# Optimization experiments

Measured on AMD Instinct MI355X. Metric: run time of the kernel, lower is better.

Reference implementation:

```python
import jax, jax.numpy as jnp
import numpy as np

B, TED, G, N, E, MD, NOISE = 10000, 512, 64, 2000, 64000, 15, 128
PAC = 10
PACDIM = (TED + NOISE) * PAC  # 6400
D0, D1 = 1024, 512


def _linear_params(k, fan_in, fan_out):
    kw, kb = jax.random.split(k)
    lim = 1.0 / np.sqrt(fan_in)
    w = jax.random.uniform(kw, (fan_in, fan_out), minval=-lim, maxval=lim, dtype=jnp.float32)
    b = jax.random.uniform(kb, (fan_out,), minval=-lim, maxval=lim, dtype=jnp.float32)
    return w, b


def setup_inputs() -> dict:
    key = jax.random.key(0)
    ks = jax.random.split(key, 12)
    inp = {
        'input_': jax.random.normal(ks[0], (B, TED), dtype=jnp.float32),
        'graphs_x': jax.random.normal(ks[1], (G, N, 1), dtype=jnp.float32),
        'edge_index': jax.random.randint(ks[2], (G, 2, E), 0, N, dtype=jnp.int32),
        'graph_ids': jax.random.randint(ks[3], (B,), 0, G, dtype=jnp.int32),
        'chain': jax.random.normal(ks[4], (B, 1), dtype=jnp.float32),
        'metadata': jax.random.normal(ks[5], (B, MD), dtype=jnp.float32),
    }
    inp['gcn_w'], inp['gcn_b'] = _linear_params(ks[6], 1, 1)
    inp['meta_w'], inp['meta_b'] = _linear_params(ks[7], 1 + MD, 32)
    inp['gme_w'], inp['gme_b'] = _linear_params(ks[8], N + 32, NOISE)
    inp['seq_w0'], inp['seq_b0'] = _linear_params(ks[9], PACDIM, D0)
    inp['seq_w1'], inp['seq_b1'] = _linear_params(ks[10], D0, D1)
    inp['seq_w2'], inp['seq_b2'] = _linear_params(ks[11], D1, 1)
    return inp


def _gcn_one(x, ei, gcn_w, gcn_b):
    # GCNConv(1,1) with self-loops and symmetric normalization.
    loops = jnp.arange(N, dtype=ei.dtype)
    src = jnp.concatenate([ei[0], loops])
    dst = jnp.concatenate([ei[1], loops])
    deg = jax.ops.segment_sum(jnp.ones_like(src, dtype=x.dtype), dst, num_segments=N)
    dinv = jax.lax.rsqrt(deg)  # deg >= 1 due to self-loops
    norm = dinv[src] * dinv[dst]  # [E+N]
    xw = x @ gcn_w  # [N,1]
    msg = xw[src] * norm[:, None]
    out = jax.ops.segment_sum(msg, dst, num_segments=N) + gcn_b
    return out.reshape(-1)  # flatten -> [N]


def reference(input_, graphs_x, edge_index, graph_ids, chain, metadata,
              gcn_w, gcn_b, meta_w, meta_b, gme_w, gme_b,
              seq_w0, seq_b0, seq_w1, seq_b1, seq_w2, seq_b2):
    # per-unique-graph GCN, vectorized over G graphs
    gcn_out = jax.vmap(lambda x, ei: _gcn_one(x, ei, gcn_w, gcn_b))(graphs_x, edge_index)  # [G,N]
    graph_emb = gcn_out[graph_ids]  # gather: [B,N]
    all_meta = jnp.concatenate([chain, metadata], axis=1)  # [B,1+MD]
    meta_emb = jax.nn.relu(all_meta @ meta_w + meta_b)  # [B,32]
    noise = jnp.concatenate([graph_emb, meta_emb], axis=1) @ gme_w + gme_b  # [B,NOISE]
    h = jnp.concatenate([input_, noise], axis=1).reshape(-1, PACDIM)  # [B/PAC, PACDIM]
    h = jax.nn.leaky_relu(h @ seq_w0 + seq_b0, 0.2)  # dropout omitted (eval mode)
    h = jax.nn.leaky_relu(h @ seq_w1 + seq_b1, 0.2)
    return h @ seq_w2 + seq_b2  # [B/PAC, 1]
```

## Files before the change

kernel.cpp:

```cpp
#include <hip/hip_runtime.h>

typedef __bf16 bf16_t;
typedef __bf16 bf16x4 __attribute__((ext_vector_type(4)));
typedef __bf16 bf16x8 __attribute__((ext_vector_type(8)));
typedef float floatx4 __attribute__((ext_vector_type(4)));

#define G_GRAPHS 64
#define N_NODES 2000
#define N_EDGES 64000
#define BATCH 10000
#define TED_ 512
#define NOISE_ 128
#define PACDIM_ 6400
#define D0_ 1024
#define D1_ 512
#define MROWS 1000
#define ESPLIT 8
#define EPB (N_EDGES / ESPLIT)

__device__ __forceinline__ void glds16(const void* g, void* l) {
    __builtin_amdgcn_global_load_lds(
        (__attribute__((address_space(1))) void*)(g),
        (__attribute__((address_space(3))) void*)(l), 16, 0, 0);
}

__global__ __launch_bounds__(256) void zero_kernel(float4* __restrict__ p, int n4) {
    int i = blockIdx.x * 256 + threadIdx.x;
    if (i < n4) p[i] = make_float4(0.f, 0.f, 0.f, 0.f);
}

__global__ __launch_bounds__(512) void deg_kernel(
    const int* __restrict__ edge_index, float* __restrict__ degs)
{
    __shared__ float h[N_NODES];
    const int g = blockIdx.y, s = blockIdx.x, tid = threadIdx.x;
    for (int n = tid; n < N_NODES; n += 512) h[n] = 0.f;
    __syncthreads();
    const int* dst = edge_index + (size_t)g * 2 * N_EDGES + N_EDGES + s * EPB;
    for (int e = tid; e < EPB; e += 512) atomicAdd(&h[dst[e]], 1.0f);
    __syncthreads();
    float* dg = degs + (size_t)g * N_NODES;
    for (int n = tid; n < N_NODES; n += 512) {
        float v = h[n];
        if (v != 0.f) atomicAdd(&dg[n], v);
    }
}

__global__ __launch_bounds__(512) void msg_kernel(
    const float* __restrict__ graphs_x, const int* __restrict__ edge_index,
    const float* __restrict__ degs, float* __restrict__ outs)
{
    __shared__ float xsl[N_NODES];
    __shared__ float dvl[N_NODES];
    __shared__ float oh[N_NODES];
    const int g = blockIdx.y, s = blockIdx.x, tid = threadIdx.x;
    const float* xg = graphs_x + (size_t)g * N_NODES;
    const float* dgg = degs + (size_t)g * N_NODES;
    for (int n = tid; n < N_NODES; n += 512) {
        xsl[n] = xg[n];
        dvl[n] = rsqrtf(dgg[n] + 1.0f);
        oh[n] = 0.f;
    }
    __syncthreads();
    const int* src = edge_index + (size_t)g * 2 * N_EDGES + s * EPB;
    const int* dst = src + N_EDGES;
    for (int e = tid; e < EPB; e += 512) {
        int ss = src[e], dd = dst[e];
        atomicAdd(&oh[dd], xsl[ss] * dvl[ss] * dvl[dd]);
    }
    __syncthreads();
    float* og = outs + (size_t)g * N_NODES;
    for (int n = tid; n < N_NODES; n += 512) {
        float v = oh[n];
        if (v != 0.f) atomicAdd(&og[n], v);
    }
}

__global__ __launch_bounds__(512) void gnoise_kernel(
    const float* __restrict__ graphs_x, const float* __restrict__ degs,
    const float* __restrict__ outs,
    const float* __restrict__ gcn_w, const float* __restrict__ gcn_b,
    const float* __restrict__ gme_w, float* __restrict__ gnoise)
{
    __shared__ float of[N_NODES];
    __shared__ float part[4][128];
    const int g = blockIdx.x, tid = threadIdx.x;
    const float w = gcn_w[0], b = gcn_b[0];
    for (int n = tid; n < N_NODES; n += 512) {
        float di2 = 1.0f / (degs[(size_t)g * N_NODES + n] + 1.0f);
        of[n] = w * (outs[(size_t)g * N_NODES + n]
                     + graphs_x[(size_t)g * N_NODES + n] * di2) + b;
    }
    __syncthreads();
    const int j = tid & 127, ch = tid >> 7;
    float acc = 0.f;
    const int n0 = ch * 500;
    for (int n = n0; n < n0 + 500; n++)
        acc += of[n] * gme_w[(size_t)n * 128 + j];
    part[ch][j] = acc;
    __syncthreads();
    if (tid < 128)
        gnoise[(size_t)g * 128 + tid] =
            part[0][tid] + part[1][tid] + part[2][tid] + part[3][tid];
}

__global__ __launch_bounds__(256) void pack_input_kernel(
    const float* __restrict__ in, bf16_t* __restrict__ A)
{
    int idx = blockIdx.x * 256 + threadIdx.x;
    if (idx >= BATCH * TED_ / 4) return;
    float4 v = ((const float4*)in)[idx];
    int b = idx >> 7;
    int c = (idx & 127) << 2;
    int r = b / 10, slot = b - r * 10;
    bf16x4 o = { (bf16_t)v.x, (bf16_t)v.y, (bf16_t)v.z, (bf16_t)v.w };
    *(bf16x4*)(A + (size_t)r * PACDIM_ + slot * 640 + c) = o;
}

__global__ __launch_bounds__(256) void meta_noise_kernel(
    const float* __restrict__ chain, const float* __restrict__ metadata,
    const int* __restrict__ graph_ids,
    const float* __restrict__ meta_w, const float* __restrict__ meta_b,
    const float* __restrict__ gme_w, const float* __restrict__ gme_b,
    const float* __restrict__ gnoise, bf16_t* __restrict__ A)
{
    int wid = (blockIdx.x * 256 + threadIdx.x) >> 6;
    int lane = threadIdx.x & 63;
    if (wid >= BATCH) return;
    const int b = wid;
    float me = 0.f;
    if (lane < 32) {
        me = meta_b[lane] + chain[b] * meta_w[lane];
        for (int i = 1; i < 16; i++)
            me += metadata[(size_t)b * 15 + (i - 1)] * meta_w[(size_t)i * 32 + lane];
        me = me > 0.f ? me : 0.f;
    }
    const int gid = graph_ids[b];
    const int j1 = lane, j2 = lane + 64;
    float n1 = gnoise[(size_t)gid * 128 + j1] + gme_b[j1];
    float n2 = gnoise[(size_t)gid * 128 + j2] + gme_b[j2];
    for (int k = 0; k < 32; k++) {
        float mk = __shfl(me, k, 64);
        const float* wrow = gme_w + (size_t)(N_NODES + k) * 128;
        n1 += mk * wrow[j1];
        n2 += mk * wrow[j2];
    }
    int r = b / 10, slot = b - r * 10;
    bf16_t* dp = A + (size_t)r * PACDIM_ + slot * 640 + TED_;
    dp[j1] = (bf16_t)n1;
    dp[j2] = (bf16_t)n2;
}

__global__ __launch_bounds__(256) void transpose_bf16_kernel(
    const float* __restrict__ W, bf16_t* __restrict__ Wt, int R, int C)
{
    __shared__ float t[32][33];
    int c0 = blockIdx.x * 32, r0 = blockIdx.y * 32;
    int tx = threadIdx.x & 31, ty = threadIdx.x >> 5;
    for (int yy = ty; yy < 32; yy += 8)
        t[yy][tx] = W[(size_t)(r0 + yy) * C + c0 + tx];
    __syncthreads();
    for (int yy = ty; yy < 32; yy += 8)
        Wt[(size_t)(c0 + yy) * R + r0 + tx] = (bf16_t)t[tx][yy];
}

__global__ __launch_bounds__(256) void gemm_bt_splitk_kernel(
    const bf16_t* __restrict__ A,
    const bf16_t* __restrict__ Bt,
    float* __restrict__ P,
    int M, int N, int K, int KS)
{
    __shared__ __align__(16) bf16_t As[128 * 32];
    __shared__ __align__(16) bf16_t Bs[128 * 32];
    const int tid = threadIdx.x;
    const int wave = tid >> 6;
    const int lane = tid & 63;
    const int mBase = blockIdx.y * 128;
    const int nBase = blockIdx.x * 128;
    const int z = blockIdx.z;
    const int Mp = gridDim.y * 128;
    const int wm = (wave & 1) * 64;
    const int wn = (wave >> 1) * 64;

    floatx4 acc[4][4] = {};

    const int c0 = tid, c1 = tid + 256;
    const int rA0 = c0 >> 2, k80 = (c0 & 3) * 8;
    const int rA1 = c1 >> 2, k81 = (c1 & 3) * 8;
    int gm0 = mBase + rA0; if (gm0 > M - 1) gm0 = M - 1;
    int gm1 = mBase + rA1; if (gm1 > M - 1) gm1 = M - 1;
    const bf16_t* aP0 = A + (size_t)gm0 * K + k80;
    const bf16_t* aP1 = A + (size_t)gm1 * K + k81;
    const bf16_t* bP0 = Bt + (size_t)(nBase + rA0) * K + k80;
    const bf16_t* bP1 = Bt + (size_t)(nBase + rA1) * K + k81;
    char* lA0 = (char*)As + wave * 1024;
    char* lA1 = (char*)As + 4096 + wave * 1024;
    char* lB0 = (char*)Bs + wave * 1024;
    char* lB1 = (char*)Bs + 4096 + wave * 1024;

    const int kq = (lane >> 4) * 8;
    const int mr = lane & 15;
    const bf16x8* ra[4]; const bf16x8* rb[4];
    for (int i = 0; i < 4; i++)
        ra[i] = (const bf16x8*)&As[(wm + i * 16 + mr) * 32 + kq];
    for (int j = 0; j < 4; j++)
        rb[j] = (const bf16x8*)&Bs[(wn + j * 16 + mr) * 32 + kq];

    const int kEnd = z * KS + KS;
    for (int k0 = z * KS; k0 < kEnd; k0 += 32) {
        __syncthreads();
        glds16(aP0 + k0, lA0);
        glds16(aP1 + k0, lA1);
        glds16(bP0 + k0, lB0);
        glds16(bP1 + k0, lB1);
        __syncthreads();
        bf16x8 af[4], bfr[4];
        for (int i = 0; i < 4; i++) af[i] = *ra[i];
        for (int j = 0; j < 4; j++) bfr[j] = *rb[j];
        for (int i = 0; i < 4; i++)
            for (int j = 0; j < 4; j++)
                acc[i][j] = __builtin_amdgcn_mfma_f32_16x16x32_bf16(
                    af[i], bfr[j], acc[i][j], 0, 0, 0);
    }

    float* Pz = P + (size_t)z * Mp * N;
    const int rq = (lane >> 4) * 4;
    const int cn = lane & 15;
    for (int j = 0; j < 4; j++) {
        int col = nBase + wn + j * 16 + cn;
        for (int i = 0; i < 4; i++)
            for (int r = 0; r < 4; r++) {
                int rowm = mBase + wm + i * 16 + rq + r;
                Pz[(size_t)rowm * N + col] = acc[i][j][r];
            }
    }
}

__global__ __launch_bounds__(256) void reduce_bias_leaky_kernel(
    const float* __restrict__ P, const float* __restrict__ bias,
    bf16_t* __restrict__ C, int M, int N, int Mp, int S)
{
    int idx = blockIdx.x * 256 + threadIdx.x;
    int total = M * (N >> 2);
    if (idx >= total) return;
    int nv = N >> 2;
    int r = idx / nv, c4 = (idx - r * nv) << 2;
    size_t off = (size_t)r * N + c4;
    size_t stride = (size_t)Mp * N;
    float4 v = *(const float4*)(P + off);
    for (int s = 1; s < S; s++) {
        float4 u = *(const float4*)(P + s * stride + off);
        v.x += u.x; v.y += u.y; v.z += u.z; v.w += u.w;
    }
    const float4 bv = *(const float4*)(bias + c4);
    v.x += bv.x; v.y += bv.y; v.z += bv.z; v.w += bv.w;
    v.x = v.x > 0.f ? v.x : 0.2f * v.x;
    v.y = v.y > 0.f ? v.y : 0.2f * v.y;
    v.z = v.z > 0.f ? v.z : 0.2f * v.z;
    v.w = v.w > 0.f ? v.w : 0.2f * v.w;
    bf16x4 o = { (bf16_t)v.x, (bf16_t)v.y, (bf16_t)v.z, (bf16_t)v.w };
    *(bf16x4*)(C + off) = o;
}

__global__ __launch_bounds__(256) void final_kernel(
    const bf16_t* __restrict__ H2, const float* __restrict__ w2,
    const float* __restrict__ b2, float* __restrict__ out)
{
    int wid = (blockIdx.x * 256 + threadIdx.x) >> 6;
    int lane = threadIdx.x & 63;
    if (wid >= MROWS) return;
    const bf16_t* row = H2 + (size_t)wid * D1_;
    float s = 0.f;
    for (int i = 0; i < 8; i++) {
        int c = i * 64 + lane;
        s += (float)row[c] * w2[c];
    }
    for (int off = 32; off; off >>= 1) s += __shfl_down(s, off, 64);
    if (lane == 0) out[wid] = s + b2[0];
}

extern "C" void kernel_launch(void* const* d_in, const int* in_sizes, int n_in,
                              void* d_out, int out_size, void* d_ws, size_t ws_size,
                              hipStream_t stream)
{
    const float* input_    = (const float*)d_in[0];
    const float* graphs_x  = (const float*)d_in[1];
    const int*   edge_idx  = (const int*)  d_in[2];
    const int*   graph_ids = (const int*)  d_in[3];
    const float* chain     = (const float*)d_in[4];
    const float* metadata  = (const float*)d_in[5];
    const float* gcn_w     = (const float*)d_in[6];
    const float* gcn_b     = (const float*)d_in[7];
    const float* meta_w    = (const float*)d_in[8];
    const float* meta_b    = (const float*)d_in[9];
    const float* gme_w     = (const float*)d_in[10];
    const float* gme_b     = (const float*)d_in[11];
    const float* seq_w0    = (const float*)d_in[12];
    const float* seq_b0    = (const float*)d_in[13];
    const float* seq_w1    = (const float*)d_in[14];
    const float* seq_b1    = (const float*)d_in[15];
    const float* seq_w2    = (const float*)d_in[16];
    const float* seq_b2    = (const float*)d_in[17];
    float* out = (float*)d_out;

    char* ws = (char*)d_ws;
    float*  gnoise = (float*)(ws + 0);
    float*  degs   = (float*)(ws + 32768);
    float*  outs   = (float*)(ws + 544768);
    bf16_t* Abuf   = (bf16_t*)(ws + 1056768);
    bf16_t* W0t    = (bf16_t*)(ws + 13856768);
    bf16_t* W1t    = (bf16_t*)(ws + 26963968);
    bf16_t* H1     = (bf16_t*)(ws + 28012544);
    bf16_t* H2     = (bf16_t*)(ws + 30060544);
    float*  P      = (float*)(ws + 31084544);

    zero_kernel<<<(2 * G_GRAPHS * N_NODES / 4 + 255) / 256, 256, 0, stream>>>(
        (float4*)degs, 2 * G_GRAPHS * N_NODES / 4);
    deg_kernel<<<dim3(ESPLIT, G_GRAPHS), 512, 0, stream>>>(edge_idx, degs);
    msg_kernel<<<dim3(ESPLIT, G_GRAPHS), 512, 0, stream>>>(graphs_x, edge_idx, degs, outs);
    gnoise_kernel<<<G_GRAPHS, 512, 0, stream>>>(graphs_x, degs, outs, gcn_w, gcn_b,
                                                gme_w, gnoise);

    pack_input_kernel<<<(BATCH * TED_ / 4 + 255) / 256, 256, 0, stream>>>(input_, Abuf);
    meta_noise_kernel<<<(BATCH * 64 + 255) / 256, 256, 0, stream>>>(
        chain, metadata, graph_ids, meta_w, meta_b, gme_w, gme_b, gnoise, Abuf);
    transpose_bf16_kernel<<<dim3(D0_ / 32, PACDIM_ / 32), 256, 0, stream>>>(
        seq_w0, W0t, PACDIM_, D0_);
    transpose_bf16_kernel<<<dim3(D1_ / 32, D0_ / 32), 256, 0, stream>>>(
        seq_w1, W1t, D0_, D1_);

    gemm_bt_splitk_kernel<<<dim3(D0_ / 128, 8, 4), 256, 0, stream>>>(
        Abuf, W0t, P, MROWS, D0_, PACDIM_, 1600);
    reduce_bias_leaky_kernel<<<(MROWS * D0_ / 4 + 255) / 256, 256, 0, stream>>>(
        P, seq_b0, H1, MROWS, D0_, 1024, 4);

    gemm_bt_splitk_kernel<<<dim3(D1_ / 128, 8, 8), 256, 0, stream>>>(
        H1, W1t, P, MROWS, D1_, D0_, 128);
    reduce_bias_leaky_kernel<<<(MROWS * D1_ / 4 + 255) / 256, 256, 0, stream>>>(
        P, seq_b1, H2, MROWS, D1_, 1024, 8);

    final_kernel<<<(MROWS * 64 + 255) / 256, 256, 0, stream>>>(H2, seq_w2, seq_b2, out);
}
```

Baseline: 302.2 us.

## Fuse small kernels, split gnoise across blocks, raise GEMM0 split-K

The gnoise projection now runs as 4 node chunks per graph and accumulates with atomics, giving more blocks and more parallelism. The input packing and meta/noise kernels are merged into one launch. The layer-1 reduce, bias and leaky ReLU are folded into the final dot-product kernel, which drops the H2 buffer. The first GEMM's split-K goes from 4 to 8. Together these cut launch count and increase parallelism, at the cost of larger partial-sum traffic and extra reads in the final kernel.

```diff
diff --git a/kernel.cpp b/kernel.cpp
--- a/kernel.cpp
+++ b/kernel.cpp
@@ -17,6 +17,8 @@
 #define MROWS 1000
 #define ESPLIT 8
 #define EPB (N_EDGES / ESPLIT)
+#define S0 8
+#define S1 8
 
 __device__ __forceinline__ void glds16(const void* g, void* l) {
     __builtin_amdgcn_global_load_lds(
@@ -76,55 +78,55 @@
     }
 }
 
-__global__ __launch_bounds__(512) void gnoise_kernel(
+__global__ __launch_bounds__(512) void gnoise_part_kernel(
     const float* __restrict__ graphs_x, const float* __restrict__ degs,
     const float* __restrict__ outs,
     const float* __restrict__ gcn_w, const float* __restrict__ gcn_b,
     const float* __restrict__ gme_w, float* __restrict__ gnoise)
 {
-    __shared__ float of[N_NODES];
+    __shared__ float of[500];
     __shared__ float part[4][128];
-    const int g = blockIdx.x, tid = threadIdx.x;
+    const int s = blockIdx.x, g = blockIdx.y, tid = threadIdx.x;
+    const int nBase = s * 500;
     const float w = gcn_w[0], b = gcn_b[0];
-    for (int n = tid; n < N_NODES; n += 512) {
-        float di2 = 1.0f / (degs[(size_t)g * N_NODES + n] + 1.0f);
-        of[n] = w * (outs[(size_t)g * N_NODES + n]
-                     + graphs_x[(size_t)g * N_NODES + n] * di2) + b;
+    for (int n = tid; n < 500; n += 512) {
+        int gn = nBase + n;
+        float di2 = 1.0f / (degs[(size_t)g * N_NODES + gn] + 1.0f);
+        of[n] = w * (outs[(size_t)g * N_NODES + gn]
+                     + graphs_x[(size_t)g * N_NODES + gn] * di2) + b;
     }
     __syncthreads();
     const int j = tid & 127, ch = tid >> 7;
     float acc = 0.f;
-    const int n0 = ch * 500;
-    for (int n = n0; n < n0 + 500; n++)
-        acc += of[n] * gme_w[(size_t)n * 128 + j];
+    const int n0 = ch * 125;
+    for (int n = n0; n < n0 + 125; n++)
+        acc += of[n] * gme_w[(size_t)(nBase + n) * 128 + j];
     part[ch][j] = acc;
     __syncthreads();
     if (tid < 128)
-        gnoise[(size_t)g * 128 + tid] =
-            part[0][tid] + part[1][tid] + part[2][tid] + part[3][tid];
-}
-
-__global__ __launch_bounds__(256) void pack_input_kernel(
-    const float* __restrict__ in, bf16_t* __restrict__ A)
-{
-    int idx = blockIdx.x * 256 + threadIdx.x;
-    if (idx >= BATCH * TED_ / 4) return;
-    float4 v = ((const float4*)in)[idx];
-    int b = idx >> 7;
-    int c = (idx & 127) << 2;
-    int r = b / 10, slot = b - r * 10;
-    bf16x4 o = { (bf16_t)v.x, (bf16_t)v.y, (bf16_t)v.z, (bf16_t)v.w };
-    *(bf16x4*)(A + (size_t)r * PACDIM_ + slot * 640 + c) = o;
-}
-
-__global__ __launch_bounds__(256) void meta_noise_kernel(
+        atomicAdd(&gnoise[(size_t)g * 128 + tid],
+                  part[0][tid] + part[1][tid] + part[2][tid] + part[3][tid]);
+}
+
+__global__ __launch_bounds__(256) void pack_meta_kernel(
+    const float* __restrict__ in,
     const float* __restrict__ chain, const float* __restrict__ metadata,
     const int* __restrict__ graph_ids,
     const float* __restrict__ meta_w, const float* __restrict__ meta_b,
     const float* __restrict__ gme_w, const float* __restrict__ gme_b,
     const float* __restrict__ gnoise, bf16_t* __restrict__ A)
 {
-    int wid = (blockIdx.x * 256 + threadIdx.x) >> 6;
+    if (blockIdx.x < 5000) {
+        int idx = blockIdx.x * 256 + threadIdx.x;
+        float4 v = ((const float4*)in)[idx];
+        int b = idx >> 7;
+        int c = (idx & 127) << 2;
+        int r = b / 10, slot = b - r * 10;
+        bf16x4 o = { (bf16_t)v.x, (bf16_t)v.y, (bf16_t)v.z, (bf16_t)v.w };
+        *(bf16x4*)(A + (size_t)r * PACDIM_ + slot * 640 + c) = o;
+        return;
+    }
+    int wid = ((blockIdx.x - 5000) * 256 + threadIdx.x) >> 6;
     int lane = threadIdx.x & 63;
     if (wid >= BATCH) return;
     const int b = wid;
@@ -262,18 +264,24 @@
     *(bf16x4*)(C + off) = o;
 }
 
-__global__ __launch_bounds__(256) void final_kernel(
-    const bf16_t* __restrict__ H2, const float* __restrict__ w2,
-    const float* __restrict__ b2, float* __restrict__ out)
+__global__ __launch_bounds__(256) void final_fused_kernel(
+    const float* __restrict__ P, const float* __restrict__ b1,
+    const float* __restrict__ w2, const float* __restrict__ b2,
+    float* __restrict__ out, int Mp, int S)
 {
     int wid = (blockIdx.x * 256 + threadIdx.x) >> 6;
     int lane = threadIdx.x & 63;
     if (wid >= MROWS) return;
-    const bf16_t* row = H2 + (size_t)wid * D1_;
+    size_t stride = (size_t)Mp * D1_;
+    const float* base = P + (size_t)wid * D1_;
     float s = 0.f;
     for (int i = 0; i < 8; i++) {
         int c = i * 64 + lane;
-        s += (float)row[c] * w2[c];
+        float v = base[c];
+        for (int z = 1; z < S; z++) v += base[(size_t)z * stride + c];
+        v += b1[c];
+        v = v > 0.f ? v : 0.2f * v;
+        s += v * w2[c];
     }
     for (int off = 32; off; off >>= 1) s += __shfl_down(s, off, 64);
     if (lane == 0) out[wid] = s + b2[0];
@@ -311,33 +319,30 @@
     bf16_t* W0t    = (bf16_t*)(ws + 13856768);
     bf16_t* W1t    = (bf16_t*)(ws + 26963968);
     bf16_t* H1     = (bf16_t*)(ws + 28012544);
-    bf16_t* H2     = (bf16_t*)(ws + 30060544);
-    float*  P      = (float*)(ws + 31084544);
-
-    zero_kernel<<<(2 * G_GRAPHS * N_NODES / 4 + 255) / 256, 256, 0, stream>>>(
-        (float4*)degs, 2 * G_GRAPHS * N_NODES / 4);
+    float*  P      = (float*)(ws + 30060544);
+
+    const int zn4 = (32768 + 512000 + 512000) / 16;
+    zero_kernel<<<(zn4 + 255) / 256, 256, 0, stream>>>((float4*)gnoise, zn4);
     deg_kernel<<<dim3(ESPLIT, G_GRAPHS), 512, 0, stream>>>(edge_idx, degs);
     msg_kernel<<<dim3(ESPLIT, G_GRAPHS), 512, 0, stream>>>(graphs_x, edge_idx, degs, outs);
-    gnoise_kernel<<<G_GRAPHS, 512, 0, stream>>>(graphs_x, degs, outs, gcn_w, gcn_b,
-                                                gme_w, gnoise);
-
-    pack_input_kernel<<<(BATCH * TED_ / 4 + 255) / 256, 256, 0, stream>>>(input_, Abuf);
-    meta_noise_kernel<<<(BATCH * 64 + 255) / 256, 256, 0, stream>>>(
-        chain, metadata, graph_ids, meta_w, meta_b, gme_w, gme_b, gnoise, Abuf);
+    gnoise_part_kernel<<<dim3(4, G_GRAPHS), 512, 0, stream>>>(
+        graphs_x, degs, outs, gcn_w, gcn_b, gme_w, gnoise);
+
+    pack_meta_kernel<<<7500, 256, 0, stream>>>(
+        input_, chain, metadata, graph_ids, meta_w, meta_b, gme_w, gme_b,
+        gnoise, Abuf);
     transpose_bf16_kernel<<<dim3(D0_ / 32, PACDIM_ / 32), 256, 0, stream>>>(
         seq_w0, W0t, PACDIM_, D0_);
     transpose_bf16_kernel<<<dim3(D1_ / 32, D0_ / 32), 256, 0, stream>>>(
         seq_w1, W1t, D0_, D1_);
 
-    gemm_bt_splitk_kernel<<<dim3(D0_ / 128, 8, 4), 256, 0, stream>>>(
-        Abuf, W0t, P, MROWS, D0_, PACDIM_, 1600);
+    gemm_bt_splitk_kernel<<<dim3(D0_ / 128, 8, S0), 256, 0, stream>>>(
+        Abuf, W0t, P, MROWS, D0_, PACDIM_, PACDIM_ / S0);
     reduce_bias_leaky_kernel<<<(MROWS * D0_ / 4 + 255) / 256, 256, 0, stream>>>(
-        P, seq_b0, H1, MROWS, D0_, 1024, 4);
-
-    gemm_bt_splitk_kernel<<<dim3(D1_ / 128, 8, 8), 256, 0, stream>>>(
-        H1, W1t, P, MROWS, D1_, D0_, 128);
-    reduce_bias_leaky_kernel<<<(MROWS * D1_ / 4 + 255) / 256, 256, 0, stream>>>(
-        P, seq_b1, H2, MROWS, D1_, 1024, 8);
-
-    final_kernel<<<(MROWS * 64 + 255) / 256, 256, 0, stream>>>(H2, seq_w2, seq_b2, out);
-}
+        P, seq_b0, H1, MROWS, D0_, 1024, S0);
+
+    gemm_bt_splitk_kernel<<<dim3(D1_ / 128, 8, S1), 256, 0, stream>>>(
+        H1, W1t, P, MROWS, D1_, D0_, D0_ / S1);
+    final_fused_kernel<<<(MROWS * 64 + 255) / 256, 256, 0, stream>>>(
+        P, seq_b1, seq_w2, seq_b2, out, 1024, S1);
+}
```

Result: faster. 276.4 us (-8.5%).
